# Kernel tuning notes

Hardware: AMD Instinct MI355X
Metric: run time of the kernel (lower is better)

The kernel has to match this reference:

```python
import jax, jax.numpy as jnp
import numpy as np

B, C, N = 2, 256, 8192
CI = 256  # inter_channels
EPS = 1e-5


def setup_inputs() -> dict:
    key = jax.random.key(0)
    ks = jax.random.split(key, 11)
    s = 1.0 / np.sqrt(C)
    si = 1.0 / np.sqrt(CI)
    return {
        "x": jax.random.normal(ks[0], (B, C, N), dtype=jnp.float32),
        "g_w": jax.random.uniform(ks[1], (CI, C), jnp.float32, -s, s),
        "g_b": jax.random.uniform(ks[2], (CI,), jnp.float32, -s, s),
        "theta_w": jax.random.uniform(ks[3], (CI, C), jnp.float32, -s, s),
        "theta_b": jax.random.uniform(ks[4], (CI,), jnp.float32, -s, s),
        "phi_w": jax.random.uniform(ks[5], (CI, C), jnp.float32, -s, s),
        "phi_b": jax.random.uniform(ks[6], (CI,), jnp.float32, -s, s),
        "w_w": jax.random.uniform(ks[7], (CI, CI), jnp.float32, -si, si),
        "w_b": jax.random.uniform(ks[8], (CI,), jnp.float32, -si, si),
        "bn_gamma": jax.random.normal(ks[9], (CI,), dtype=jnp.float32),
        "bn_beta": jax.random.normal(ks[10], (CI,), dtype=jnp.float32),
    }


def reference(x, g_w, g_b, theta_w, theta_b, phi_w, phi_b, w_w, w_b, bn_gamma, bn_beta):
    # 1x1 Conv1d == channel-wise linear: (o,c) @ (b,c,n) -> (b,o,n)
    g_x = jnp.einsum('oc,bcn->bno', g_w, x) + g_b            # (b, n, ci)
    theta_x = jnp.einsum('oc,bcn->bno', theta_w, x) + theta_b  # (b, n, ci)
    phi_x = jnp.einsum('oc,bcn->bon', phi_w, x) + phi_b[:, None]  # (b, ci, n)
    f = jnp.einsum('bnc,bcm->bnm', theta_x, phi_x)           # (b, n, n), unscaled
    f_div_C = jax.nn.softmax(f, axis=-1)
    y = jnp.einsum('bnm,bmc->bcn', f_div_C, g_x)             # (b, ci, n)
    # W: 1x1 conv then BatchNorm1d (training-mode batch statistics)
    z = jnp.einsum('oc,bcn->bon', w_w, y) + w_b[:, None]     # (b, ci, n)
    mean = jnp.mean(z, axis=(0, 2), keepdims=True)
    var = jnp.mean(jnp.square(z - mean), axis=(0, 2), keepdims=True)  # biased var
    z_hat = (z - mean) * jax.lax.rsqrt(var + EPS)
    out = bn_gamma[:, None] * z_hat + bn_beta[:, None]
    return out
```

## Files before the change

kernel.cpp:

```cpp
#include <hip/hip_runtime.h>
#include <hip/hip_bf16.h>
#include <stdint.h>

#define BB  2
#define CC  256
#define NN  8192
#define CIc 256
#define LOG2E 1.4426950408889634f

typedef __attribute__((ext_vector_type(4)))  float f32x4;
typedef __attribute__((ext_vector_type(16))) float f32x16;
typedef __attribute__((ext_vector_type(8)))  short s16x8;
typedef __attribute__((ext_vector_type(4)))  short s16x4;
typedef __attribute__((ext_vector_type(4)))  int   i32x4;
typedef __attribute__((ext_vector_type(2)))  int   i32x2;

static __device__ __forceinline__ short f2bf(float f) {
    union { float f; unsigned u; } v; v.f = f;
    unsigned r = (v.u + 0x7FFFu + ((v.u >> 16) & 1u)) >> 16;
    return (short)r;
}
static __device__ __forceinline__ float bf2f(short h) {
    union { unsigned u; float f; } v; v.u = ((unsigned)(unsigned short)h) << 16;
    return v.f;
}

static __device__ __forceinline__ void gload16(const void* g, void* l) {
    __builtin_amdgcn_global_load_lds(
        (const __attribute__((address_space(1))) unsigned int*)g,
        (__attribute__((address_space(3))) unsigned int*)l, 16, 0, 0);
}

__global__ __launch_bounds__(256) void pack_kernel(
    const float* __restrict__ tw, const float* __restrict__ pw,
    const float* __restrict__ gw, const float* __restrict__ ww,
    short* __restrict__ Wf)
{
    int gid  = blockIdx.x * 256 + threadIdx.x;
    int lane = gid & 63;
    int grp  = gid >> 6;
    int ks = grp & 7, ot = (grp >> 3) & 15, m = grp >> 7;
    const float* W = (m == 0) ? tw : (m == 1) ? pw : (m == 2) ? gw : ww;
    const float* p = &W[(size_t)(ot * 16 + (lane & 15)) * 256 + ks * 32 + (lane >> 4) * 8];
    float4 a = *(const float4*)p, c = *(const float4*)(p + 4);
    s16x8 o;
    o[0] = f2bf(a.x); o[1] = f2bf(a.y); o[2] = f2bf(a.z); o[3] = f2bf(a.w);
    o[4] = f2bf(c.x); o[5] = f2bf(c.y); o[6] = f2bf(c.z); o[7] = f2bf(c.w);
    *(s16x8*)&Wf[(size_t)gid * 8] = o;
}

__global__ __launch_bounds__(256) void proj_kernel(
    const float* __restrict__ x, const short* __restrict__ Wf,
    const float* __restrict__ tb, const float* __restrict__ pb,
    const float* __restrict__ gb,
    short* __restrict__ Qf, short* __restrict__ Kf, short* __restrict__ Vf)
{
    __shared__ char xls[64 * 512];
    const int blk = blockIdx.x;
    const int m   = blk % 3;
    const int r2  = blk / 3;
    const int b   = r2 >> 7;
    const int n0  = (r2 & 127) << 6;
    const int tid = threadIdx.x;

    for (int it = 0; it < 16; ++it) {
        int chunk = it * 256 + tid;
        int c  = chunk >> 4;
        int n4 = (chunk & 15) << 2;
        const float4 v = *(const float4*)&x[((size_t)b * CC + c) * NN + n0 + n4];
        float vv[4] = {v.x, v.y, v.z, v.w};
        #pragma unroll
        for (int j = 0; j < 4; ++j) {
            int row = n4 + j;
            int addr = row * 512 + ((c * 2) ^ ((row & 31) << 4));
            *(short*)(xls + addr) = f2bf(vv[j]);
        }
    }
    __syncthreads();

    const int lane = tid & 63, w = tid >> 6;
    const int lo = lane & 15, g = lane >> 4;

    s16x8 bfr[8];
    #pragma unroll
    for (int k = 0; k < 8; ++k) {
        int row = w * 16 + lo;
        int addr = row * 512 + ((k * 64 + g * 16) ^ ((row & 31) << 4));
        bfr[k] = *(const s16x8*)(xls + addr);
    }

    const float* bias = (m == 0) ? tb : (m == 1) ? pb : gb;
    const size_t wfm = (size_t)m * 16 * 8 * 512;

    for (int ot = 0; ot < 16; ++ot) {
        s16x8 afr[8];
        #pragma unroll
        for (int k = 0; k < 8; ++k)
            afr[k] = *(const s16x8*)&Wf[wfm + (size_t)(ot * 8 + k) * 512 + lane * 8];
        f32x4 acc = {0.f, 0.f, 0.f, 0.f};
        if (m < 2) {
            #pragma unroll
            for (int k = 0; k < 8; ++k)
                acc = __builtin_amdgcn_mfma_f32_16x16x32_bf16(afr[k], bfr[k], acc, 0, 0, 0);
        } else {
            #pragma unroll
            for (int k = 0; k < 8; ++k)
                acc = __builtin_amdgcn_mfma_f32_16x16x32_bf16(bfr[k], afr[k], acc, 0, 0, 0);
        }

        if (m < 2) {
            const float4 bi = *(const float4*)&bias[ot * 16 + g * 4];
            const float sc = (m == 0) ? LOG2E : 1.0f;
            short* O = (m == 0) ? Qf : Kf;
            int n = n0 + w * 16 + lo;
            s16x4 st;
            st[0] = f2bf((acc[0] + bi.x) * sc);
            st[1] = f2bf((acc[1] + bi.y) * sc);
            st[2] = f2bf((acc[2] + bi.z) * sc);
            st[3] = f2bf((acc[3] + bi.w) * sc);
            size_t a = ((((size_t)b * 256 + (n >> 5)) * 16 + ot) * 64
                        + (n & 31) + 32 * (g >> 1)) * 8 + (g & 1) * 4;
            *(s16x4*)&O[a] = st;
        } else {
            int nb = n0 + w * 16 + g * 4;
            int o  = ot * 16 + lo;
            float bo = bias[o];
            s16x4 st;
            st[0] = f2bf(acc[0] + bo);
            st[1] = f2bf(acc[1] + bo);
            st[2] = f2bf(acc[2] + bo);
            st[3] = f2bf(acc[3] + bo);
            size_t a = ((((size_t)b * 256 + (nb >> 5)) * 16 + (w & 1) * 8 + (ot >> 1)) * 64
                        + (ot & 1) * 16 + lo + 32 * (g >> 1)) * 8 + (g & 1) * 4;
            *(s16x4*)&Vf[a] = st;
        }
    }
}

template<int SPLIT>
__global__ __launch_bounds__(256, 2) void attn6_kernel(
    const short* __restrict__ Qf, const short* __restrict__ Kf,
    const short* __restrict__ Vf,
    short* __restrict__ part,
    float* __restrict__ ml)
{
    __shared__ char lds[65536];
    const int blk   = blockIdx.x;
    const int combo = blk & (2 * SPLIT - 1);
    const int split = combo >> 1;
    const int b     = combo & 1;
    const int qblk  = blk / (2 * SPLIT);
    const int tid = threadIdx.x, lane = tid & 63, w = tid >> 6;
    const int l31 = lane & 31, h = lane >> 5;
    const size_t bN = (size_t)b * NN;
    const int tgbase = (split * (NN / SPLIT)) >> 5;
    const int NT = (NN / SPLIT) / 32;

    #pragma unroll
    for (int j = 0; j < 8; ++j) {
        const int inst = w * 8 + j;
        if (inst < 16)
            gload16(&Kf[(((size_t)(b * 256 + tgbase) * 16) + inst) * 512 + lane * 8],
                    lds + inst * 1024);
        else
            gload16(&Vf[(((size_t)(b * 256 + tgbase) * 16) + (inst - 16)) * 512 + lane * 8],
                    lds + 16384 + (inst - 16) * 1024);
    }

    s16x8 qf[16];
    {
        const int qtg = qblk * 4 + w;
        #pragma unroll
        for (int ks = 0; ks < 16; ++ks)
            qf[ks] = *(const s16x8*)&Qf[(((size_t)(b * 256 + qtg) * 16) + ks) * 512 + lane * 8];
    }

    f32x16 acc[8];
    #pragma unroll
    for (int dt = 0; dt < 8; ++dt)
        #pragma unroll
        for (int r = 0; r < 16; ++r) acc[dt][r] = 0.f;
    float l_run = 0.f;

    for (int t = 0; t < NT; ++t) {
        __syncthreads();
        const char* cbuf = lds + (t & 1) * 32768;
        const int tg = tgbase + t;
        if (t + 1 < NT) {
            char* nbuf = lds + ((t + 1) & 1) * 32768;
            #pragma unroll
            for (int j = 0; j < 8; ++j) {
                const int inst = w * 8 + j;
                if (inst < 16)
                    gload16(&Kf[(((size_t)(b * 256 + tg + 1) * 16) + inst) * 512 + lane * 8],
                            nbuf + inst * 1024);
                else
                    gload16(&Vf[(((size_t)(b * 256 + tg + 1) * 16) + (inst - 16)) * 512 + lane * 8],
                            nbuf + 16384 + (inst - 16) * 1024);
            }
        }

        f32x16 sacc;
        #pragma unroll
        for (int r = 0; r < 16; ++r) sacc[r] = 0.f;
        __builtin_amdgcn_s_setprio(1);
        #pragma unroll
        for (int ks = 0; ks < 16; ++ks) {
            s16x8 kf = *(const s16x8*)(cbuf + ks * 1024 + lane * 16);
            sacc = __builtin_amdgcn_mfma_f32_32x32x16_bf16(kf, qf[ks], sacc, 0, 0, 0);
        }
        __builtin_amdgcn_s_setprio(0);

        float sum = 0.f;
        #pragma unroll
        for (int r = 0; r < 16; ++r) {
            float p = exp2f(sacc[r]);
            sacc[r] = p; sum += p;
        }
        l_run += sum;

        union { int wd[4]; s16x8 v; } f0, f1;
        {
            int w01, w23, w45, w67;
            asm("v_cvt_pk_bf16_f32 %0, %1, %2" : "=v"(w01) : "v"(sacc[0]), "v"(sacc[1]));
            asm("v_cvt_pk_bf16_f32 %0, %1, %2" : "=v"(w23) : "v"(sacc[2]), "v"(sacc[3]));
            asm("v_cvt_pk_bf16_f32 %0, %1, %2" : "=v"(w45) : "v"(sacc[4]), "v"(sacc[5]));
            asm("v_cvt_pk_bf16_f32 %0, %1, %2" : "=v"(w67) : "v"(sacc[6]), "v"(sacc[7]));
            i32x2 r02 = __builtin_amdgcn_permlane32_swap(w01, w45, false, false);
            i32x2 r13 = __builtin_amdgcn_permlane32_swap(w23, w67, false, false);
            f0.wd[0] = r02[0]; f0.wd[1] = r13[0];
            f0.wd[2] = r02[1]; f0.wd[3] = r13[1];
        }
        {
            int w01, w23, w45, w67;
            asm("v_cvt_pk_bf16_f32 %0, %1, %2" : "=v"(w01) : "v"(sacc[8]),  "v"(sacc[9]));
            asm("v_cvt_pk_bf16_f32 %0, %1, %2" : "=v"(w23) : "v"(sacc[10]), "v"(sacc[11]));
            asm("v_cvt_pk_bf16_f32 %0, %1, %2" : "=v"(w45) : "v"(sacc[12]), "v"(sacc[13]));
            asm("v_cvt_pk_bf16_f32 %0, %1, %2" : "=v"(w67) : "v"(sacc[14]), "v"(sacc[15]));
            i32x2 r02 = __builtin_amdgcn_permlane32_swap(w01, w45, false, false);
            i32x2 r13 = __builtin_amdgcn_permlane32_swap(w23, w67, false, false);
            f1.wd[0] = r02[0]; f1.wd[1] = r13[0];
            f1.wd[2] = r02[1]; f1.wd[3] = r13[1];
        }

        const char* vbuf = cbuf + 16384;
        __builtin_amdgcn_s_setprio(1);
        #pragma unroll
        for (int dt = 0; dt < 8; ++dt) {
            s16x8 v0 = *(const s16x8*)(vbuf + (dt) * 1024 + lane * 16);
            s16x8 v1 = *(const s16x8*)(vbuf + (8 + dt) * 1024 + lane * 16);
            acc[dt] = __builtin_amdgcn_mfma_f32_32x32x16_bf16(v0, f0.v, acc[dt], 0, 0, 0);
            acc[dt] = __builtin_amdgcn_mfma_f32_32x32x16_bf16(v1, f1.v, acc[dt], 0, 0, 0);
        }
        __builtin_amdgcn_s_setprio(0);
    }

    const int qb = qblk * 4 + w;
    const size_t pb2 = (((size_t)(split * 2 + b) * 256 + qb) * 32) * 256;
    #pragma unroll
    for (int dt = 0; dt < 8; ++dt)
        #pragma unroll
        for (int rg = 0; rg < 4; ++rg) {
            s16x4 st;
            st[0] = f2bf(acc[dt][rg * 4 + 0]);
            st[1] = f2bf(acc[dt][rg * 4 + 1]);
            st[2] = f2bf(acc[dt][rg * 4 + 2]);
            st[3] = f2bf(acc[dt][rg * 4 + 3]);
            *(s16x4*)&part[pb2 + (size_t)(dt * 4 + rg) * 256 + lane * 4] = st;
        }
    float lf = l_run + __shfl_xor(l_run, 32);
    if (h == 0) {
        size_t mi = ((size_t)split * (BB * NN) + bN + qb * 32 + l31) * 2;
        ml[mi] = 0.f; ml[mi + 1] = lf;
    }
}

template<int SPLIT>
__global__ __launch_bounds__(256) void combine2_kernel(
    const short* __restrict__ part, const float* __restrict__ ml,
    short* __restrict__ yp)
{
    int gid  = blockIdx.x * 256 + threadIdx.x;
    int lane = gid & 63;
    int slot = (gid >> 6) & 31;
    int qb   = (gid >> 11) & 255;
    int b    = gid >> 19;
    int dt = slot >> 2, rg = slot & 3;
    int l31 = lane & 31, h = lane >> 5;
    int q = qb * 32 + l31;

    float mm[SPLIT], ll[SPLIT];
    float m = -1e30f;
    #pragma unroll
    for (int s = 0; s < SPLIT; ++s) {
        mm[s] = ml[((size_t)s * (BB * NN) + (size_t)b * NN + q) * 2];
        ll[s] = ml[((size_t)s * (BB * NN) + (size_t)b * NN + q) * 2 + 1];
        m = fmaxf(m, mm[s]);
    }
    float den = 0.f, a[SPLIT];
    #pragma unroll
    for (int s = 0; s < SPLIT; ++s) { a[s] = __expf(mm[s] - m); den += a[s] * ll[s]; }
    float o[4] = {0.f, 0.f, 0.f, 0.f};
    #pragma unroll
    for (int s = 0; s < SPLIT; ++s) {
        s16x4 p = *(const s16x4*)&part[((((size_t)(s * 2 + b) * 256 + qb) * 32 + slot) * 64 + lane) * 4];
        #pragma unroll
        for (int j = 0; j < 4; ++j) o[j] += a[s] * bf2f(p[j]);
    }
    float inv = 1.f / den;
    s16x4 st;
    #pragma unroll
    for (int j = 0; j < 4; ++j) st[j] = f2bf(o[j] * inv);
    size_t a2 = ((((size_t)b * 512 + (q >> 4)) * 8 + dt) * 64 + (q & 15) + rg * 16) * 8 + h * 4;
    *(s16x4*)&yp[a2] = st;
}

template<int SPLIT>
__global__ __launch_bounds__(256) void zgemm_fused_kernel(
    const short* __restrict__ part, const float* __restrict__ ml,
    const short* __restrict__ Wf, const float* __restrict__ wb,
    float* __restrict__ z)
{
    const int blk = blockIdx.x;
    const int b   = blk >> 7;
    const int n0  = (blk & 127) << 6;
    const int tid = threadIdx.x;
    const int lane = tid & 63, w = tid >> 6, lo = lane & 15, g = lane >> 4;
    const int q  = n0 + w * 16 + lo;
    const int qb = q >> 5, l31 = q & 31;

    float mm[SPLIT], ll[SPLIT], a[SPLIT];
    float m = -1e30f;
    #pragma unroll
    for (int s = 0; s < SPLIT; ++s) {
        mm[s] = ml[((size_t)s * (BB * NN) + (size_t)b * NN + q) * 2];
        ll[s] = ml[((size_t)s * (BB * NN) + (size_t)b * NN + q) * 2 + 1];
        m = fmaxf(m, mm[s]);
    }
    float den = 0.f;
    #pragma unroll
    for (int s = 0; s < SPLIT; ++s) { a[s] = __expf(mm[s] - m); den += a[s] * ll[s]; }
    float inv = 1.f / den;
    #pragma unroll
    for (int s = 0; s < SPLIT; ++s) a[s] *= inv;

    s16x8 afr[8];
    #pragma unroll
    for (int k = 0; k < 8; ++k) {
        float o[8] = {0.f, 0.f, 0.f, 0.f, 0.f, 0.f, 0.f, 0.f};
        #pragma unroll
        for (int s = 0; s < SPLIT; ++s) {
            size_t base = ((((size_t)(s * 2 + b) * 256 + qb) * 32 + (k * 4 + g)) * 64 + l31) * 4;
            s16x4 plo = *(const s16x4*)&part[base];
            s16x4 phi = *(const s16x4*)&part[base + 128];
            #pragma unroll
            for (int j = 0; j < 4; ++j) {
                o[j]     += a[s] * bf2f(plo[j]);
                o[4 + j] += a[s] * bf2f(phi[j]);
            }
        }
        #pragma unroll
        for (int j = 0; j < 8; ++j) afr[k][j] = f2bf(o[j]);
    }

    for (int ot = 0; ot < 16; ++ot) {
        f32x4 acc = {0.f, 0.f, 0.f, 0.f};
        #pragma unroll
        for (int k = 0; k < 8; ++k) {
            s16x8 bfr = *(const s16x8*)&Wf[(size_t)((3 * 16 + ot) * 8 + k) * 512 + lane * 8];
            acc = __builtin_amdgcn_mfma_f32_16x16x32_bf16(afr[k], bfr, acc, 0, 0, 0);
        }
        float bias = wb[ot * 16 + lo];
        float4 st = {acc[0] + bias, acc[1] + bias, acc[2] + bias, acc[3] + bias};
        *(float4*)&z[((size_t)b * CIc + ot * 16 + lo) * NN + n0 + w * 16 + g * 4] = st;
    }
}

__global__ __launch_bounds__(256) void zgemm_kernel(
    const short* __restrict__ yp, const short* __restrict__ Wf,
    const float* __restrict__ wb, float* __restrict__ z)
{
    const int blk = blockIdx.x;
    const int b   = blk >> 7;
    const int n0  = (blk & 127) << 6;
    const int tid = threadIdx.x;
    const int lane = tid & 63, w = tid >> 6, lo = lane & 15, g = lane >> 4;

    s16x8 afr[8];
    #pragma unroll
    for (int k = 0; k < 8; ++k)
        afr[k] = *(const s16x8*)&yp[((((size_t)b * 512 + (n0 >> 4) + w) * 8 + k) * 64 + lane) * 8];

    for (int ot = 0; ot < 16; ++ot) {
        f32x4 acc = {0.f, 0.f, 0.f, 0.f};
        #pragma unroll
        for (int k = 0; k < 8; ++k) {
            s16x8 bfr = *(const s16x8*)&Wf[(size_t)((3 * 16 + ot) * 8 + k) * 512 + lane * 8];
            acc = __builtin_amdgcn_mfma_f32_16x16x32_bf16(afr[k], bfr, acc, 0, 0, 0);
        }
        float bias = wb[ot * 16 + lo];
        float4 st = {acc[0] + bias, acc[1] + bias, acc[2] + bias, acc[3] + bias};
        *(float4*)&z[((size_t)b * CIc + ot * 16 + lo) * NN + n0 + w * 16 + g * 4] = st;
    }
}

__global__ __launch_bounds__(256) void bn_kernel(
    float* __restrict__ z,
    const float* __restrict__ gamma, const float* __restrict__ beta)
{
    const int o = blockIdx.x;
    const int tid = threadIdx.x;
    float4 v[16];
    float s = 0.f, s2 = 0.f;
    #pragma unroll
    for (int b2 = 0; b2 < BB; ++b2) {
        float* row = &z[((size_t)b2 * CIc + o) * NN];
        #pragma unroll
        for (int i = 0; i < 8; ++i) {
            float4 t = *(const float4*)&row[(i * 256 + tid) * 4];
            v[b2 * 8 + i] = t;
            s  += t.x + t.y + t.z + t.w;
            s2 += t.x * t.x + t.y * t.y + t.z * t.z + t.w * t.w;
        }
    }
    #pragma unroll
    for (int off = 1; off < 64; off <<= 1) {
        s  += __shfl_xor(s, off);
        s2 += __shfl_xor(s2, off);
    }
    __shared__ float rs[8];
    if ((tid & 63) == 0) { rs[tid >> 6] = s; rs[4 + (tid >> 6)] = s2; }
    __syncthreads();
    float S  = rs[0] + rs[1] + rs[2] + rs[3];
    float S2 = rs[4] + rs[5] + rs[6] + rs[7];
    float mean = S / (float)(BB * NN);
    float var  = S2 / (float)(BB * NN) - mean * mean;
    float rsq  = rsqrtf(var + 1e-5f);
    float ga = gamma[o], be = beta[o];
    float sc = rsq * ga, of = be - mean * rsq * ga;
    #pragma unroll
    for (int b2 = 0; b2 < BB; ++b2) {
        float* row = &z[((size_t)b2 * CIc + o) * NN];
        #pragma unroll
        for (int i = 0; i < 8; ++i) {
            float4 t = v[b2 * 8 + i];
            t.x = t.x * sc + of;
            t.y = t.y * sc + of;
            t.z = t.z * sc + of;
            t.w = t.w * sc + of;
            *(float4*)&row[(i * 256 + tid) * 4] = t;
        }
    }
}

extern "C" void kernel_launch(void* const* d_in, const int* in_sizes, int n_in,
                              void* d_out, int out_size, void* d_ws, size_t ws_size,
                              hipStream_t stream) {
    const float* x    = (const float*)d_in[0];
    const float* g_w  = (const float*)d_in[1];
    const float* g_b  = (const float*)d_in[2];
    const float* th_w = (const float*)d_in[3];
    const float* th_b = (const float*)d_in[4];
    const float* ph_w = (const float*)d_in[5];
    const float* ph_b = (const float*)d_in[6];
    const float* w_w  = (const float*)d_in[7];
    const float* w_b  = (const float*)d_in[8];
    const float* bn_g = (const float*)d_in[9];
    const float* bn_b = (const float*)d_in[10];

    char* ws = (char*)d_ws;
    short* Qf    = (short*)ws;
    short* Kf    = (short*)(ws + 8  * 1048576);
    short* Vf    = (short*)(ws + 16 * 1048576);
    float* ml    = (float*)(ws + 24 * 1048576);
    short* Wfb   = (short*)(ws + 25 * 1048576);
    float* z     = (float*)d_out;

    const size_t need4 = (size_t)26 * 1048576 + (size_t)4 * BB * NN * CIc * 2;
    const bool  big    = ws_size >= need4;

    pack_kernel<<<128, 256, 0, stream>>>(th_w, ph_w, g_w, w_w, Wfb);
    proj_kernel<<<768, 256, 0, stream>>>(x, Wfb, th_b, ph_b, g_b, Qf, Kf, Vf);

    if (big) {
        short* part = (short*)(ws + 26 * 1048576);
        attn6_kernel<4><<<512, 256, 0, stream>>>(Qf, Kf, Vf, part, ml);
        zgemm_fused_kernel<4><<<256, 256, 0, stream>>>(part, ml, Wfb, w_b, z);
    } else {
        short* part = (short*)d_out;
        attn6_kernel<2><<<256, 256, 0, stream>>>(Qf, Kf, Vf, part, ml);
        combine2_kernel<2><<<4096, 256, 0, stream>>>(part, ml, Qf);
        zgemm_kernel<<<256, 256, 0, stream>>>(Qf, Wfb, w_b, z);
    }

    bn_kernel<<<256, 256, 0, stream>>>(z, bn_g, bn_b);
}
```

Measured before the change: 201.6 us.

## Fuse BN statistics into zgemm epilogue and merge projection blocks

After: 226.1 us. +12.2%, slower.

```diff
diff --git a/kernel.cpp b/kernel.cpp
--- a/kernel.cpp
+++ b/kernel.cpp
@@ -57,10 +57,8 @@
 {
     __shared__ char xls[64 * 512];
     const int blk = blockIdx.x;
-    const int m   = blk % 3;
-    const int r2  = blk / 3;
-    const int b   = r2 >> 7;
-    const int n0  = (r2 & 127) << 6;
+    const int b   = blk >> 7;
+    const int n0  = (blk & 127) << 6;
     const int tid = threadIdx.x;
 
     for (int it = 0; it < 16; ++it) {
@@ -89,50 +87,52 @@
         bfr[k] = *(const s16x8*)(xls + addr);
     }
 
-    const float* bias = (m == 0) ? tb : (m == 1) ? pb : gb;
-    const size_t wfm = (size_t)m * 16 * 8 * 512;
-
-    for (int ot = 0; ot < 16; ++ot) {
-        s16x8 afr[8];
-        #pragma unroll
-        for (int k = 0; k < 8; ++k)
-            afr[k] = *(const s16x8*)&Wf[wfm + (size_t)(ot * 8 + k) * 512 + lane * 8];
-        f32x4 acc = {0.f, 0.f, 0.f, 0.f};
-        if (m < 2) {
+    for (int m = 0; m < 3; ++m) {
+        const float* bias = (m == 0) ? tb : (m == 1) ? pb : gb;
+        const size_t wfm = (size_t)m * 16 * 8 * 512;
+
+        for (int ot = 0; ot < 16; ++ot) {
+            s16x8 afr[8];
             #pragma unroll
             for (int k = 0; k < 8; ++k)
-                acc = __builtin_amdgcn_mfma_f32_16x16x32_bf16(afr[k], bfr[k], acc, 0, 0, 0);
-        } else {
-            #pragma unroll
-            for (int k = 0; k < 8; ++k)
-                acc = __builtin_amdgcn_mfma_f32_16x16x32_bf16(bfr[k], afr[k], acc, 0, 0, 0);
-        }
-
-        if (m < 2) {
-            const float4 bi = *(const float4*)&bias[ot * 16 + g * 4];
-            const float sc = (m == 0) ? LOG2E : 1.0f;
-            short* O = (m == 0) ? Qf : Kf;
-            int n = n0 + w * 16 + lo;
-            s16x4 st;
-            st[0] = f2bf((acc[0] + bi.x) * sc);
-            st[1] = f2bf((acc[1] + bi.y) * sc);
-            st[2] = f2bf((acc[2] + bi.z) * sc);
-            st[3] = f2bf((acc[3] + bi.w) * sc);
-            size_t a = ((((size_t)b * 256 + (n >> 5)) * 16 + ot) * 64
-                        + (n & 31) + 32 * (g >> 1)) * 8 + (g & 1) * 4;
-            *(s16x4*)&O[a] = st;
-        } else {
-            int nb = n0 + w * 16 + g * 4;
-            int o  = ot * 16 + lo;
-            float bo = bias[o];
-            s16x4 st;
-            st[0] = f2bf(acc[0] + bo);
-            st[1] = f2bf(acc[1] + bo);
-            st[2] = f2bf(acc[2] + bo);
-            st[3] = f2bf(acc[3] + bo);
-            size_t a = ((((size_t)b * 256 + (nb >> 5)) * 16 + (w & 1) * 8 + (ot >> 1)) * 64
-                        + (ot & 1) * 16 + lo + 32 * (g >> 1)) * 8 + (g & 1) * 4;
-            *(s16x4*)&Vf[a] = st;
+                afr[k] = *(const s16x8*)&Wf[wfm + (size_t)(ot * 8 + k) * 512 + lane * 8];
+            f32x4 acc = {0.f, 0.f, 0.f, 0.f};
+            if (m < 2) {
+                #pragma unroll
+                for (int k = 0; k < 8; ++k)
+                    acc = __builtin_amdgcn_mfma_f32_16x16x32_bf16(afr[k], bfr[k], acc, 0, 0, 0);
+            } else {
+                #pragma unroll
+                for (int k = 0; k < 8; ++k)
+                    acc = __builtin_amdgcn_mfma_f32_16x16x32_bf16(bfr[k], afr[k], acc, 0, 0, 0);
+            }
+
+            if (m < 2) {
+                const float4 bi = *(const float4*)&bias[ot * 16 + g * 4];
+                const float sc = (m == 0) ? LOG2E : 1.0f;
+                short* O = (m == 0) ? Qf : Kf;
+                int n = n0 + w * 16 + lo;
+                s16x4 st;
+                st[0] = f2bf((acc[0] + bi.x) * sc);
+                st[1] = f2bf((acc[1] + bi.y) * sc);
+                st[2] = f2bf((acc[2] + bi.z) * sc);
+                st[3] = f2bf((acc[3] + bi.w) * sc);
+                size_t a = ((((size_t)b * 256 + (n >> 5)) * 16 + ot) * 64
+                            + (n & 31) + 32 * (g >> 1)) * 8 + (g & 1) * 4;
+                *(s16x4*)&O[a] = st;
+            } else {
+                int nb = n0 + w * 16 + g * 4;
+                int o  = ot * 16 + lo;
+                float bo = bias[o];
+                s16x4 st;
+                st[0] = f2bf(acc[0] + bo);
+                st[1] = f2bf(acc[1] + bo);
+                st[2] = f2bf(acc[2] + bo);
+                st[3] = f2bf(acc[3] + bo);
+                size_t a = ((((size_t)b * 256 + (nb >> 5)) * 16 + (w & 1) * 8 + (ot >> 1)) * 64
+                            + (ot & 1) * 16 + lo + 32 * (g >> 1)) * 8 + (g & 1) * 4;
+                *(s16x4*)&Vf[a] = st;
+            }
         }
     }
 }
@@ -319,8 +319,9 @@
 __global__ __launch_bounds__(256) void zgemm_fused_kernel(
     const short* __restrict__ part, const float* __restrict__ ml,
     const short* __restrict__ Wf, const float* __restrict__ wb,
-    float* __restrict__ z)
-{
+    float* __restrict__ z, float* __restrict__ bnpart)
+{
+    __shared__ float bnp[4][256][2];
     const int blk = blockIdx.x;
     const int b   = blk >> 7;
     const int n0  = (blk & 127) << 6;
@@ -373,7 +374,18 @@
         float bias = wb[ot * 16 + lo];
         float4 st = {acc[0] + bias, acc[1] + bias, acc[2] + bias, acc[3] + bias};
         *(float4*)&z[((size_t)b * CIc + ot * 16 + lo) * NN + n0 + w * 16 + g * 4] = st;
-    }
+
+        float s1 = st.x + st.y + st.z + st.w;
+        float s2 = st.x * st.x + st.y * st.y + st.z * st.z + st.w * st.w;
+        s1 += __shfl_xor(s1, 16); s2 += __shfl_xor(s2, 16);
+        s1 += __shfl_xor(s1, 32); s2 += __shfl_xor(s2, 32);
+        if (g == 0) { bnp[w][ot * 16 + lo][0] = s1; bnp[w][ot * 16 + lo][1] = s2; }
+    }
+    __syncthreads();
+    float S1 = bnp[0][tid][0] + bnp[1][tid][0] + bnp[2][tid][0] + bnp[3][tid][0];
+    float S2 = bnp[0][tid][1] + bnp[1][tid][1] + bnp[2][tid][1] + bnp[3][tid][1];
+    bnpart[((size_t)tid * 256 + blk) * 2]     = S1;
+    bnpart[((size_t)tid * 256 + blk) * 2 + 1] = S2;
 }
 
 __global__ __launch_bounds__(256) void zgemm_kernel(
@@ -401,6 +413,44 @@
         float bias = wb[ot * 16 + lo];
         float4 st = {acc[0] + bias, acc[1] + bias, acc[2] + bias, acc[3] + bias};
         *(float4*)&z[((size_t)b * CIc + ot * 16 + lo) * NN + n0 + w * 16 + g * 4] = st;
+    }
+}
+
+__global__ __launch_bounds__(256) void bn_apply_kernel(
+    float* __restrict__ z, const float* __restrict__ bnpart,
+    const float* __restrict__ gamma, const float* __restrict__ beta)
+{
+    const int o = blockIdx.x;
+    const int tid = threadIdx.x;
+    float s  = bnpart[((size_t)o * 256 + tid) * 2];
+    float s2 = bnpart[((size_t)o * 256 + tid) * 2 + 1];
+    #pragma unroll
+    for (int off = 1; off < 64; off <<= 1) {
+        s  += __shfl_xor(s, off);
+        s2 += __shfl_xor(s2, off);
+    }
+    __shared__ float rs[8];
+    if ((tid & 63) == 0) { rs[tid >> 6] = s; rs[4 + (tid >> 6)] = s2; }
+    __syncthreads();
+    float S  = rs[0] + rs[1] + rs[2] + rs[3];
+    float S2 = rs[4] + rs[5] + rs[6] + rs[7];
+    float mean = S / (float)(BB * NN);
+    float var  = S2 / (float)(BB * NN) - mean * mean;
+    float rsq  = rsqrtf(var + 1e-5f);
+    float ga = gamma[o], be = beta[o];
+    float sc = rsq * ga, of = be - mean * rsq * ga;
+    #pragma unroll
+    for (int b2 = 0; b2 < BB; ++b2) {
+        float* row = &z[((size_t)b2 * CIc + o) * NN];
+        #pragma unroll
+        for (int i = 0; i < 8; ++i) {
+            float4 t = *(const float4*)&row[(i * 256 + tid) * 4];
+            t.x = t.x * sc + of;
+            t.y = t.y * sc + of;
+            t.z = t.z * sc + of;
+            t.w = t.w * sc + of;
+            *(float4*)&row[(i * 256 + tid) * 4] = t;
+        }
     }
 }
 
@@ -474,24 +524,25 @@
     short* Vf    = (short*)(ws + 16 * 1048576);
     float* ml    = (float*)(ws + 24 * 1048576);
     short* Wfb   = (short*)(ws + 25 * 1048576);
+    float* bnp   = (float*)(ws + 25 * 1048576 + 524288);
     float* z     = (float*)d_out;
 
     const size_t need4 = (size_t)26 * 1048576 + (size_t)4 * BB * NN * CIc * 2;
     const bool  big    = ws_size >= need4;
 
     pack_kernel<<<128, 256, 0, stream>>>(th_w, ph_w, g_w, w_w, Wfb);
-    proj_kernel<<<768, 256, 0, stream>>>(x, Wfb, th_b, ph_b, g_b, Qf, Kf, Vf);
+    proj_kernel<<<256, 256, 0, stream>>>(x, Wfb, th_b, ph_b, g_b, Qf, Kf, Vf);
 
     if (big) {
         short* part = (short*)(ws + 26 * 1048576);
         attn6_kernel<4><<<512, 256, 0, stream>>>(Qf, Kf, Vf, part, ml);
-        zgemm_fused_kernel<4><<<256, 256, 0, stream>>>(part, ml, Wfb, w_b, z);
+        zgemm_fused_kernel<4><<<256, 256, 0, stream>>>(part, ml, Wfb, w_b, z, bnp);
+        bn_apply_kernel<<<256, 256, 0, stream>>>(z, bnp, bn_g, bn_b);
     } else {
         short* part = (short*)d_out;
         attn6_kernel<2><<<256, 256, 0, stream>>>(Qf, Kf, Vf, part, ml);
         combine2_kernel<2><<<4096, 256, 0, stream>>>(part, ml, Qf);
         zgemm_kernel<<<256, 256, 0, stream>>>(Qf, Wfb, w_b, z);
-    }
-
-    bn_kernel<<<256, 256, 0, stream>>>(z, bn_g, bn_b);
-}
+        bn_kernel<<<256, 256, 0, stream>>>(z, bn_g, bn_b);
+    }
+}
```
